# Performance work log

Measured on AMD Instinct MI355X. Metric: run time of the kernel, lower is better.

The kernel has to match this reference:

```python
import jax, jax.numpy as jnp
import numpy as np
from jax import lax

B_, L_, D_, N_, K_ = 2, 4096, 1024, 16, 4


def setup_inputs() -> dict:
    key = jax.random.key(0)
    ks = jax.random.split(key, 11)
    s = lambda fan: 1.0 / np.sqrt(fan)
    return {
        "x": jax.random.normal(ks[0], (B_, L_, D_), jnp.float32),
        "W_in": jax.random.normal(ks[1], (D_, 2 * D_), jnp.float32) * s(D_),
        "b_in": jax.random.normal(ks[2], (2 * D_,), jnp.float32) * 0.01,
        "conv_w": jax.random.normal(ks[3], (D_, K_), jnp.float32) * s(K_),
        "conv_b": jax.random.normal(ks[4], (D_,), jnp.float32) * 0.01,
        "W_x": jax.random.normal(ks[5], (D_, 2 * N_), jnp.float32) * s(D_),
        "b_x": jax.random.normal(ks[6], (2 * N_,), jnp.float32) * 0.01,
        "A_log": jax.random.normal(ks[7], (D_, N_), jnp.float32),
        "D_param": jnp.ones((D_,), jnp.float32),
        "W_out": jax.random.normal(ks[8], (D_, D_), jnp.float32) * s(D_),
        "b_out": jax.random.normal(ks[9], (D_,), jnp.float32) * 0.01,
    }


def silu(x):
    return x * jax.nn.sigmoid(x)


def s6_forward(x, W_in, b_in, conv_w, conv_b, W_x, b_x, A_log, D_param, W_out, b_out):
    b, L, D = x.shape
    # in_proj then split into ssm stream and gate
    x_and_gate = x @ W_in + b_in                      # [b, L, 2D]
    x_ssm, gate = jnp.split(x_and_gate, 2, axis=-1)   # each [b, L, D]

    # depthwise causal conv: padding=(d_conv-1, d_conv-1) then [:, :, :L] == left-pad only
    xc = jnp.transpose(x_ssm, (0, 2, 1))              # [b, D, L]
    xc = lax.conv_general_dilated(
        xc, conv_w[:, None, :],                       # [D, 1, K]
        window_strides=(1,), padding=[(K_ - 1, 0)],
        feature_group_count=D,
        dimension_numbers=("NCH", "OIH", "NCH"),
    ) + conv_b[None, :, None]
    x_conv = silu(jnp.transpose(xc, (0, 2, 1)))       # [b, L, D]

    # data-dependent B, C
    BC = x_conv @ W_x + b_x                           # [b, L, 2N]
    B_mat, C_mat = jnp.split(BC, 2, axis=-1)          # each [b, L, N]

    A_discrete = jnp.exp(-jnp.exp(A_log))             # [D, N]

    # sequential selective scan over L, carry h: [b, D, N]
    def step(h, inp):
        xc_t, B_t, C_t = inp                          # [b,D], [b,N], [b,N]
        h = A_discrete[None] * h + xc_t[:, :, None] * B_t[:, None, :]
        y = jnp.einsum("bn,bdn->bd", C_t, h) + D_param * xc_t
        return h, y

    h0 = jnp.zeros((b, D, N_), x.dtype)
    xs = (jnp.transpose(x_conv, (1, 0, 2)),
          jnp.transpose(B_mat, (1, 0, 2)),
          jnp.transpose(C_mat, (1, 0, 2)))
    h_final, ys = lax.scan(step, h0, xs)              # ys: [L, b, D]
    y = jnp.transpose(ys, (1, 0, 2))                  # [b, L, D]

    y = y * silu(gate)
    y = y @ W_out + b_out
    final_state = h_final.mean(axis=1)                # [b, N]
    return y, final_state


def reference(x, W_in, b_in, conv_w, conv_b, W_x, b_x, A_log, D_param, W_out, b_out):
    return s6_forward(x, W_in, b_in, conv_w, conv_b, W_x, b_x, A_log, D_param, W_out, b_out)
```

## Files before the change

kernel.cpp:

```cpp
#include <hip/hip_runtime.h>
#include <hip/hip_bf16.h>
#include <math.h>

#define LL 4096
#define DD 1024
#define NN 16
#define KK 4
#define BB 2
#define MM (BB * LL)
#define NC 128
#define LC 32

typedef unsigned short ushort_t;
typedef short s16x8 __attribute__((ext_vector_type(8)));
typedef float f32x4 __attribute__((ext_vector_type(4)));
typedef unsigned int u32;

__device__ __forceinline__ ushort_t f2bf(float f) {
  __hip_bfloat16 h = __float2bfloat16(f);
  return *reinterpret_cast<ushort_t*>(&h);
}
__device__ __forceinline__ float bf2f(ushort_t u) {
  union { u32 i; float f; } c;
  c.i = ((u32)u) << 16;
  return c.f;
}

template <bool BF16OUT>
__global__ __launch_bounds__(256) void gemm_bt_mfma(
    const ushort_t* __restrict__ A,
    const ushort_t* __restrict__ BT,
    const float* __restrict__ bias,
    void* __restrict__ Cv, int N) {
  constexpr int K = 1024;
  __shared__ ushort_t As[128 * 64];
  __shared__ ushort_t Bs[128 * 64];

  const int tid = threadIdx.x;
  const int lane = tid & 63;
  const int w = tid >> 6;
  const int wm = w & 1, wn = w >> 1;
  const int row0 = blockIdx.y * 128;
  const int col0 = blockIdx.x * 128;

  const int lrow8 = lane >> 3;
  const int lkc = (lane & 7) ^ lrow8;

  f32x4 acc[4][4];
#pragma unroll
  for (int i = 0; i < 4; ++i)
#pragma unroll
    for (int j = 0; j < 4; ++j) acc[i][j] = (f32x4){0.f, 0.f, 0.f, 0.f};

  const int frow = lane & 15;
  const int quad = lane >> 4;
  const int r7 = frow & 7;

  for (int k0 = 0; k0 < K; k0 += 64) {
#pragma unroll
    for (int it = 0; it < 4; ++it) {
      int r = it * 32 + w * 8;
      __builtin_amdgcn_global_load_lds(
          (const __attribute__((address_space(1))) u32*)(A + (size_t)(row0 + r + lrow8) * K + k0 + lkc * 8),
          (__attribute__((address_space(3))) u32*)(As + r * 64), 16, 0, 0);
      __builtin_amdgcn_global_load_lds(
          (const __attribute__((address_space(1))) u32*)(BT + (size_t)(col0 + r + lrow8) * K + k0 + lkc * 8),
          (__attribute__((address_space(3))) u32*)(Bs + r * 64), 16, 0, 0);
    }
    __syncthreads();

#pragma unroll
    for (int half = 0; half < 2; ++half) {
      s16x8 af[4], bf[4];
#pragma unroll
      for (int mi = 0; mi < 4; ++mi)
        af[mi] = *(const s16x8*)&As[(wm * 64 + mi * 16 + frow) * 64 +
                                    (((half * 4 + quad) ^ r7) * 8)];
#pragma unroll
      for (int ni = 0; ni < 4; ++ni)
        bf[ni] = *(const s16x8*)&Bs[(wn * 64 + ni * 16 + frow) * 64 +
                                    (((half * 4 + quad) ^ r7) * 8)];
#pragma unroll
      for (int mi = 0; mi < 4; ++mi)
#pragma unroll
        for (int ni = 0; ni < 4; ++ni)
          acc[mi][ni] = __builtin_amdgcn_mfma_f32_16x16x32_bf16(
              af[mi], bf[ni], acc[mi][ni], 0, 0, 0);
    }
    __syncthreads();
  }

#pragma unroll
  for (int mi = 0; mi < 4; ++mi) {
#pragma unroll
    for (int ni = 0; ni < 4; ++ni) {
      int col = col0 + wn * 64 + ni * 16 + frow;
      float b = bias[col];
#pragma unroll
      for (int r = 0; r < 4; ++r) {
        int row = row0 + wm * 64 + mi * 16 + quad * 4 + r;
        if constexpr (BF16OUT)
          ((ushort_t*)Cv)[(size_t)row * N + col] = f2bf(acc[mi][ni][r] + b);
        else
          ((float*)Cv)[(size_t)row * N + col] = acc[mi][ni][r] + b;
      }
    }
  }
}

__global__ __launch_bounds__(128) void bc_mfma_k(
    const ushort_t* __restrict__ A, const ushort_t* __restrict__ BT,
    const float* __restrict__ bias, float* __restrict__ C) {
  constexpr int K = 1024;
  __shared__ ushort_t As[32 * 32];
  __shared__ ushort_t Bs[32 * 32];

  const int tid = threadIdx.x;
  const int lane = tid & 63;
  const int w = tid >> 6;
  const int row0 = blockIdx.x * 32;
  const int lrow = lane >> 2;
  const int lkc = (lane & 3) ^ ((lrow >> 1) & 3);
  const int frow = lane & 15;
  const int quad = lane >> 4;
  const int sw = (frow >> 1) & 3;

  f32x4 acc[2];
  acc[0] = (f32x4){0.f, 0.f, 0.f, 0.f};
  acc[1] = (f32x4){0.f, 0.f, 0.f, 0.f};

  for (int k0 = 0; k0 < K; k0 += 32) {
    __builtin_amdgcn_global_load_lds(
        (const __attribute__((address_space(1))) u32*)(A + (size_t)(row0 + w * 16 + lrow) * K + k0 + lkc * 8),
        (__attribute__((address_space(3))) u32*)(As + (w * 16) * 32), 16, 0, 0);
    __builtin_amdgcn_global_load_lds(
        (const __attribute__((address_space(1))) u32*)(BT + (size_t)(w * 16 + lrow) * K + k0 + lkc * 8),
        (__attribute__((address_space(3))) u32*)(Bs + (w * 16) * 32), 16, 0, 0);
    __syncthreads();

    s16x8 af = *(const s16x8*)&As[(w * 16 + frow) * 32 + (quad ^ sw) * 8];
    s16x8 bf0 = *(const s16x8*)&Bs[(frow)*32 + (quad ^ sw) * 8];
    s16x8 bf1 = *(const s16x8*)&Bs[(16 + frow) * 32 + (quad ^ sw) * 8];
    acc[0] = __builtin_amdgcn_mfma_f32_16x16x32_bf16(af, bf0, acc[0], 0, 0, 0);
    acc[1] = __builtin_amdgcn_mfma_f32_16x16x32_bf16(af, bf1, acc[1], 0, 0, 0);
    __syncthreads();
  }

#pragma unroll
  for (int ni = 0; ni < 2; ++ni) {
    int col = ni * 16 + frow;
    float b = bias[col];
#pragma unroll
    for (int r = 0; r < 4; ++r) {
      int row = row0 + w * 16 + quad * 4 + r;
      C[(size_t)row * 32 + col] = acc[ni][r] + b;
    }
  }
}

__global__ __launch_bounds__(256) void prep_k(
    const float* __restrict__ x, ushort_t* __restrict__ Xb,
    float* __restrict__ fs, const float* __restrict__ W_in,
    const float* __restrict__ W_out, const float* __restrict__ W_x,
    ushort_t* __restrict__ WinT, ushort_t* __restrict__ WoutT,
    ushort_t* __restrict__ WxT, const float* __restrict__ A_log,
    float* __restrict__ Adis, float* __restrict__ ALC) {
  constexpr int K = 1024;
  const int tid = threadIdx.x;
  if (blockIdx.z == 0) {
    if (blockIdx.x == 0 && blockIdx.y == 0 && tid < 32) fs[tid] = 0.f;
    int i = (blockIdx.y * 64 + blockIdx.x) * 256 + tid;
    float4 v = ((const float4*)x)[i];
    ushort4 o;
    o.x = f2bf(v.x); o.y = f2bf(v.y); o.z = f2bf(v.z); o.w = f2bf(v.w);
    ((ushort4*)Xb)[i] = o;
    return;
  }
  int by = blockIdx.y;
  if (by >= 96) {
    if (by >= 104 || blockIdx.x != 0) return;
    int base = (by - 96) * 2048 + tid * 8;
#pragma unroll
    for (int j = 0; j < 8; ++j) {
      float e = __expf(A_log[base + j]);
      Adis[base + j] = __expf(-e);
      ALC[base + j] = __expf(-(float)LC * e);
    }
    return;
  }
  const float* W;
  ushort_t* WT;
  int N;
  if (by < 32) {
    W = W_in; WT = WinT; N = 2048;
  } else if (by < 64) {
    if (blockIdx.x >= 32) return;
    W = W_out; WT = WoutT; N = 1024;
    by -= 32;
  } else {
    if (blockIdx.x >= 1) return;
    W = W_x; WT = WxT; N = 32;
    by -= 64;
  }
  __shared__ float t[32][33];
  int nb = blockIdx.x * 32, kb = by * 32;
  int tx = tid & 31, ty = tid >> 5;
#pragma unroll
  for (int i = 0; i < 32; i += 8)
    t[ty + i][tx] = W[(size_t)(kb + ty + i) * N + nb + tx];
  __syncthreads();
#pragma unroll
  for (int i = 0; i < 32; i += 8)
    WT[(size_t)(nb + ty + i) * K + kb + tx] = f2bf(t[tx][ty + i]);
}

__global__ __launch_bounds__(256) void conv_silu_k(
    const ushort_t* __restrict__ XGb, const float* __restrict__ conv_w,
    const float* __restrict__ conv_b, ushort_t* __restrict__ XCb) {
  __shared__ float cw[128 * 33];
  const int tid = threadIdx.x;
#pragma unroll
  for (int j = 0; j < 4; ++j) {
    int d = tid + j * 256;
    float4 v = ((const float4*)conv_w)[d];
    float* p = &cw[(d >> 3) * 33 + (d & 7) * 4];
    p[0] = v.x; p[1] = v.y; p[2] = v.z; p[3] = v.w;
  }
  __syncthreads();

  int gid = blockIdx.x * 256 + tid;
  int m = gid >> 7;
  int dg = gid & 127;
  int d0 = dg * 8;
  int l = m & (LL - 1);
  const float* w = &cw[dg * 33];

  float4 b0 = ((const float4*)conv_b)[dg * 2];
  float4 b1 = ((const float4*)conv_b)[dg * 2 + 1];
  float acc[8] = {b0.x, b0.y, b0.z, b0.w, b1.x, b1.y, b1.z, b1.w};

#pragma unroll
  for (int k = 0; k < KK; ++k) {
    int li = l + k - (KK - 1);
    if (li < 0) continue;
    s16x8 v = *(const s16x8*)(XGb + (size_t)(m + k - (KK - 1)) * 2048 + d0);
#pragma unroll
    for (int j = 0; j < 8; ++j)
      acc[j] += bf2f((ushort_t)v[j]) * w[j * 4 + k];
  }
  ushort_t o[8];
#pragma unroll
  for (int j = 0; j < 8; ++j) {
    float s = acc[j] / (1.f + __expf(-acc[j]));
    o[j] = f2bf(s);
  }
  *(s16x8*)(XCb + (size_t)m * DD + d0) = *(const s16x8*)o;
}

__global__ __launch_bounds__(256) void scan_local_k(
    const ushort_t* __restrict__ XCb, const float* __restrict__ BC,
    const float* __restrict__ Adis, float* __restrict__ S) {
  const int b = blockIdx.x;
  const int w = threadIdx.x >> 6;
  const int lane = threadIdx.x & 63;
  const int c = blockIdx.y * 4 + w;
  const int d0 = blockIdx.z * 128 + lane * 2;
  const int t0 = c * LC;
  const size_t rowb = (size_t)b * LL;

  __shared__ float bcs_all[4][LC * 32];
  float* bcs = bcs_all[w];
  {
    const float4* src = (const float4*)(BC + (rowb + t0) * 32);
    float4* dst = (float4*)bcs;
#pragma unroll
    for (int i = 0; i < 4; ++i) dst[lane + i * 64] = src[lane + i * 64];
  }
  f32x4 av[8];
#pragma unroll
  for (int i = 0; i < 8; ++i) av[i] = *(const f32x4*)(Adis + d0 * 16 + i * 4);

  float h0[NN], h1[NN];
#pragma unroll
  for (int n = 0; n < NN; ++n) { h0[n] = 0.f; h1[n] = 0.f; }

  const ushort_t* xp = XCb + (rowb + t0) * DD + d0;
  u32 xw = *(const u32*)xp;
  for (int t = 0; t < LC; ++t) {
    u32 xw_n = (t + 1 < LC) ? *(const u32*)(xp + (size_t)(t + 1) * DD) : 0u;
    float x0 = bf2f((ushort_t)(xw & 0xffff));
    float x1 = bf2f((ushort_t)(xw >> 16));
    const float* bp = bcs + t * 32;
#pragma unroll
    for (int n = 0; n < NN; ++n) {
      float bv = bp[n];
      h0[n] = av[n >> 2][n & 3] * h0[n] + x0 * bv;
      h1[n] = av[4 + (n >> 2)][n & 3] * h1[n] + x1 * bv;
    }
    xw = xw_n;
  }
  float* sp = S + ((size_t)(b * NC + c) * NN) * DD + d0;
#pragma unroll
  for (int n = 0; n < NN; ++n) {
    float2 v = {h0[n], h1[n]};
    *(float2*)(sp + (size_t)n * DD) = v;
  }
}

__global__ __launch_bounds__(256) void scan_carry_k(
    float* __restrict__ S, const float* __restrict__ ALC,
    float* __restrict__ fs) {
  const int idx = blockIdx.x * 256 + threadIdx.x;
  const int d = idx & (DD - 1);
  const int n = (idx >> 10) & (NN - 1);
  const int b = idx >> 14;

  const float aLC = ALC[d * NN + n];
  float h = 0.f;
  for (int c = 0; c < NC; ++c) {
    size_t off = ((size_t)(b * NC + c) * NN + n) * DD + d;
    float s = S[off];
    S[off] = h;
    h = aLC * h + s;
  }
  __shared__ float red[256];
  red[threadIdx.x] = h;
  __syncthreads();
#pragma unroll
  for (int s2 = 128; s2 > 0; s2 >>= 1) {
    if (threadIdx.x < s2) red[threadIdx.x] += red[threadIdx.x + s2];
    __syncthreads();
  }
  if (threadIdx.x == 0) atomicAdd(&fs[b * NN + n], red[0] * (1.f / (float)DD));
}

__global__ __launch_bounds__(256) void scan_final_k(
    const ushort_t* __restrict__ XCb, const ushort_t* __restrict__ XGb,
    const float* __restrict__ BC, const float* __restrict__ Adis,
    const float* __restrict__ D_param, const float* __restrict__ H0,
    ushort_t* __restrict__ Y1b) {
  const int b = blockIdx.x;
  const int w = threadIdx.x >> 6;
  const int lane = threadIdx.x & 63;
  const int c = blockIdx.y * 4 + w;
  const int d0 = blockIdx.z * 128 + lane * 2;
  const int t0 = c * LC;
  const size_t rowb = (size_t)b * LL;

  __shared__ float bcs_all[4][LC * 32];
  float* bcs = bcs_all[w];
  {
    const float4* src = (const float4*)(BC + (rowb + t0) * 32);
    float4* dst = (float4*)bcs;
#pragma unroll
    for (int i = 0; i < 4; ++i) dst[lane + i * 64] = src[lane + i * 64];
  }
  f32x4 av[8];
#pragma unroll
  for (int i = 0; i < 8; ++i) av[i] = *(const f32x4*)(Adis + d0 * 16 + i * 4);

  float h0[NN], h1[NN];
  const float* hp = H0 + ((size_t)(b * NC + c) * NN) * DD + d0;
#pragma unroll
  for (int n = 0; n < NN; ++n) {
    float2 v = *(const float2*)(hp + (size_t)n * DD);
    h0[n] = v.x;
    h1[n] = v.y;
  }
  float2 Dp = *(const float2*)(D_param + d0);

  const ushort_t* xp = XCb + (rowb + t0) * DD + d0;
  const ushort_t* gp = XGb + (rowb + t0) * 2048 + DD + d0;
  ushort_t* yp = Y1b + (rowb + t0) * DD + d0;
  u32 xw = *(const u32*)xp;
  u32 gw = *(const u32*)gp;
  for (int t = 0; t < LC; ++t) {
    u32 xw_n = 0u, gw_n = 0u;
    if (t + 1 < LC) {
      xw_n = *(const u32*)(xp + (size_t)(t + 1) * DD);
      gw_n = *(const u32*)(gp + (size_t)(t + 1) * 2048);
    }
    float x0 = bf2f((ushort_t)(xw & 0xffff));
    float x1 = bf2f((ushort_t)(xw >> 16));
    float g0 = bf2f((ushort_t)(gw & 0xffff));
    float g1 = bf2f((ushort_t)(gw >> 16));
    float y0 = Dp.x * x0, y1 = Dp.y * x1;
    const float* bp = bcs + t * 32;
#pragma unroll
    for (int n = 0; n < NN; ++n) {
      float bv = bp[n], cv = bp[16 + n];
      h0[n] = av[n >> 2][n & 3] * h0[n] + x0 * bv;
      h1[n] = av[4 + (n >> 2)][n & 3] * h1[n] + x1 * bv;
      y0 += cv * h0[n];
      y1 += cv * h1[n];
    }
    float sg0 = g0 / (1.f + __expf(-g0));
    float sg1 = g1 / (1.f + __expf(-g1));
    u32 outw = (u32)f2bf(y0 * sg0) | ((u32)f2bf(y1 * sg1) << 16);
    *(u32*)(yp + (size_t)t * DD) = outw;
    xw = xw_n;
    gw = gw_n;
  }
}

extern "C" void kernel_launch(void* const* d_in, const int* in_sizes, int n_in,
                              void* d_out, int out_size, void* d_ws,
                              size_t ws_size, hipStream_t stream) {
  const float* x = (const float*)d_in[0];
  const float* W_in = (const float*)d_in[1];
  const float* b_in = (const float*)d_in[2];
  const float* conv_w = (const float*)d_in[3];
  const float* conv_b = (const float*)d_in[4];
  const float* W_x = (const float*)d_in[5];
  const float* b_x = (const float*)d_in[6];
  const float* A_log = (const float*)d_in[7];
  const float* D_param = (const float*)d_in[8];
  const float* W_out = (const float*)d_in[9];
  const float* b_out = (const float*)d_in[10];
  float* out = (float*)d_out;
  float* fs = out + (size_t)MM * DD;

  float* BC = (float*)d_ws;
  float* S = BC + (size_t)MM * 32;
  float* Adis = S + (size_t)BB * NC * NN * DD;
  float* ALC = Adis + (size_t)DD * NN;
  ushort_t* Xb = (ushort_t*)(ALC + (size_t)DD * NN);
  ushort_t* XGb = Xb + (size_t)MM * DD;
  ushort_t* XCb = XGb + (size_t)MM * 2048;
  ushort_t* Y1b = XCb + (size_t)MM * DD;
  ushort_t* WinT = Y1b + (size_t)MM * DD;
  ushort_t* WoutT = WinT + (size_t)2048 * DD;
  ushort_t* WxT = WoutT + (size_t)DD * DD;

  dim3 blk(256);
  prep_k<<<dim3(64, 128, 2), blk, 0, stream>>>(x, Xb, fs, W_in, W_out, W_x,
                                               WinT, WoutT, WxT, A_log, Adis,
                                               ALC);
  gemm_bt_mfma<true><<<dim3(2048 / 128, MM / 128), blk, 0, stream>>>(
      Xb, WinT, b_in, XGb, 2048);
  conv_silu_k<<<dim3((MM * 128) / 256), blk, 0, stream>>>(XGb, conv_w, conv_b,
                                                          XCb);
  bc_mfma_k<<<dim3(MM / 32), dim3(128), 0, stream>>>(XCb, WxT, b_x, BC);
  scan_local_k<<<dim3(BB, NC / 4, DD / 128), blk, 0, stream>>>(XCb, BC, Adis,
                                                               S);
  scan_carry_k<<<dim3((BB * DD * NN) / 256), blk, 0, stream>>>(S, ALC, fs);
  scan_final_k<<<dim3(BB, NC / 4, DD / 128), blk, 0, stream>>>(
      XCb, XGb, BC, Adis, D_param, S, Y1b);
  gemm_bt_mfma<false><<<dim3(1024 / 128, MM / 128), blk, 0, stream>>>(
      Y1b, WoutT, b_out, out, 1024);
}
```

Before: 249.7 us.

## Fuse causal conv+SiLU into BC GEMM and scan kernels, drop XCb buffer

Removes the standalone conv_silu kernel and the bf16 XCb intermediate. The BC projection kernel now computes conv+SiLU on the fly into LDS before its MFMA, and both scan kernels recompute conv+SiLU from XGb using a sliding 4-tap register window. This cuts one launch and a write plus several reads of an 8M×bf16 buffer, at the cost of redundant conv arithmetic and strided loads from the wider XGb rows. The carry scan also prefetches the next chunk value.

```diff
diff --git a/kernel.cpp b/kernel.cpp
--- a/kernel.cpp
+++ b/kernel.cpp
@@ -24,6 +24,9 @@
   union { u32 i; float f; } c;
   c.i = ((u32)u) << 16;
   return c.f;
+}
+__device__ __forceinline__ float silu(float v) {
+  return v / (1.f + __expf(-v));
 }
 
 template <bool BF16OUT>
@@ -108,53 +111,91 @@
   }
 }
 
-__global__ __launch_bounds__(128) void bc_mfma_k(
-    const ushort_t* __restrict__ A, const ushort_t* __restrict__ BT,
-    const float* __restrict__ bias, float* __restrict__ C) {
+__global__ __launch_bounds__(256) void convbc_k(
+    const ushort_t* __restrict__ XGb,
+    const float* __restrict__ conv_w,
+    const float* __restrict__ conv_b,
+    const ushort_t* __restrict__ WxT,
+    const float* __restrict__ b_x,
+    float* __restrict__ BC) {
   constexpr int K = 1024;
-  __shared__ ushort_t As[32 * 32];
-  __shared__ ushort_t Bs[32 * 32];
+  __shared__ ushort_t As[32 * 64];
+  __shared__ ushort_t Bs[32 * 64];
+  __shared__ float cw[128 * 33];
+  __shared__ float cb[1024];
 
   const int tid = threadIdx.x;
   const int lane = tid & 63;
   const int w = tid >> 6;
+  const int wm = w & 1, wn = w >> 1;
   const int row0 = blockIdx.x * 32;
-  const int lrow = lane >> 2;
-  const int lkc = (lane & 3) ^ ((lrow >> 1) & 3);
+  const int l0 = row0 & (LL - 1);
+
+#pragma unroll
+  for (int j = 0; j < 4; ++j) {
+    int d = tid + j * 256;
+    float4 v = ((const float4*)conv_w)[d];
+    float* p = &cw[(d >> 3) * 33 + (d & 7) * 4];
+    p[0] = v.x; p[1] = v.y; p[2] = v.z; p[3] = v.w;
+    cb[d] = conv_b[d];
+  }
+  __syncthreads();
+
+  const int r = tid >> 3;
+  const int o = tid & 7;
+  const int l = l0 + r;
   const int frow = lane & 15;
   const int quad = lane >> 4;
-  const int sw = (frow >> 1) & 3;
-
-  f32x4 acc[2];
-  acc[0] = (f32x4){0.f, 0.f, 0.f, 0.f};
-  acc[1] = (f32x4){0.f, 0.f, 0.f, 0.f};
-
-  for (int k0 = 0; k0 < K; k0 += 32) {
+  const int lkc = (lane & 7) ^ (lane >> 3);
+
+  f32x4 acc = (f32x4){0.f, 0.f, 0.f, 0.f};
+
+  for (int kk = 0; kk < K; kk += 64) {
+    const ushort_t* xb = XGb + (size_t)(row0 + r) * 2048 + kk + o * 8;
+    s16x8 v[4];
+#pragma unroll
+    for (int k = 0; k < 4; ++k) {
+      if (l + k - 3 >= 0)
+        v[k] = *(const s16x8*)(xb + (ptrdiff_t)(k - 3) * 2048);
+      else
+        v[k] = (s16x8){0, 0, 0, 0, 0, 0, 0, 0};
+    }
+    const int dg = (kk >> 3) + o;
+    const float* wp = &cw[dg * 33];
+    float a8[8];
+#pragma unroll
+    for (int j = 0; j < 8; ++j) a8[j] = cb[kk + o * 8 + j];
+#pragma unroll
+    for (int k = 0; k < 4; ++k)
+#pragma unroll
+      for (int j = 0; j < 8; ++j)
+        a8[j] += bf2f((ushort_t)v[k][j]) * wp[j * 4 + k];
+    ushort_t pk[8];
+#pragma unroll
+    for (int j = 0; j < 8; ++j) pk[j] = f2bf(silu(a8[j]));
+    *(s16x8*)&As[r * 64 + (o ^ (r & 7)) * 8] = *(const s16x8*)pk;
+
     __builtin_amdgcn_global_load_lds(
-        (const __attribute__((address_space(1))) u32*)(A + (size_t)(row0 + w * 16 + lrow) * K + k0 + lkc * 8),
-        (__attribute__((address_space(3))) u32*)(As + (w * 16) * 32), 16, 0, 0);
-    __builtin_amdgcn_global_load_lds(
-        (const __attribute__((address_space(1))) u32*)(BT + (size_t)(w * 16 + lrow) * K + k0 + lkc * 8),
-        (__attribute__((address_space(3))) u32*)(Bs + (w * 16) * 32), 16, 0, 0);
+        (const __attribute__((address_space(1))) u32*)(WxT + (size_t)(w * 8 + (lane >> 3)) * 1024 + kk + lkc * 8),
+        (__attribute__((address_space(3))) u32*)(Bs + (w * 8 + (lane >> 3)) * 64), 16, 0, 0);
     __syncthreads();
 
-    s16x8 af = *(const s16x8*)&As[(w * 16 + frow) * 32 + (quad ^ sw) * 8];
-    s16x8 bf0 = *(const s16x8*)&Bs[(frow)*32 + (quad ^ sw) * 8];
-    s16x8 bf1 = *(const s16x8*)&Bs[(16 + frow) * 32 + (quad ^ sw) * 8];
-    acc[0] = __builtin_amdgcn_mfma_f32_16x16x32_bf16(af, bf0, acc[0], 0, 0, 0);
-    acc[1] = __builtin_amdgcn_mfma_f32_16x16x32_bf16(af, bf1, acc[1], 0, 0, 0);
+#pragma unroll
+    for (int s = 0; s < 2; ++s) {
+      int slot = ((s * 4 + quad) ^ (frow & 7)) * 8;
+      s16x8 af = *(const s16x8*)&As[(wm * 16 + frow) * 64 + slot];
+      s16x8 bf = *(const s16x8*)&Bs[(wn * 16 + frow) * 64 + slot];
+      acc = __builtin_amdgcn_mfma_f32_16x16x32_bf16(af, bf, acc, 0, 0, 0);
+    }
     __syncthreads();
   }
 
-#pragma unroll
-  for (int ni = 0; ni < 2; ++ni) {
-    int col = ni * 16 + frow;
-    float b = bias[col];
-#pragma unroll
-    for (int r = 0; r < 4; ++r) {
-      int row = row0 + w * 16 + quad * 4 + r;
-      C[(size_t)row * 32 + col] = acc[ni][r] + b;
-    }
+  int col = wn * 16 + frow;
+  float b = b_x[col];
+#pragma unroll
+  for (int rr = 0; rr < 4; ++rr) {
+    int row = row0 + wm * 16 + quad * 4 + rr;
+    BC[(size_t)row * 32 + col] = acc[rr] + b;
   }
 }
 
@@ -214,52 +255,10 @@
     WT[(size_t)(nb + ty + i) * K + kb + tx] = f2bf(t[tx][ty + i]);
 }
 
-__global__ __launch_bounds__(256) void conv_silu_k(
-    const ushort_t* __restrict__ XGb, const float* __restrict__ conv_w,
-    const float* __restrict__ conv_b, ushort_t* __restrict__ XCb) {
-  __shared__ float cw[128 * 33];
-  const int tid = threadIdx.x;
-#pragma unroll
-  for (int j = 0; j < 4; ++j) {
-    int d = tid + j * 256;
-    float4 v = ((const float4*)conv_w)[d];
-    float* p = &cw[(d >> 3) * 33 + (d & 7) * 4];
-    p[0] = v.x; p[1] = v.y; p[2] = v.z; p[3] = v.w;
-  }
-  __syncthreads();
-
-  int gid = blockIdx.x * 256 + tid;
-  int m = gid >> 7;
-  int dg = gid & 127;
-  int d0 = dg * 8;
-  int l = m & (LL - 1);
-  const float* w = &cw[dg * 33];
-
-  float4 b0 = ((const float4*)conv_b)[dg * 2];
-  float4 b1 = ((const float4*)conv_b)[dg * 2 + 1];
-  float acc[8] = {b0.x, b0.y, b0.z, b0.w, b1.x, b1.y, b1.z, b1.w};
-
-#pragma unroll
-  for (int k = 0; k < KK; ++k) {
-    int li = l + k - (KK - 1);
-    if (li < 0) continue;
-    s16x8 v = *(const s16x8*)(XGb + (size_t)(m + k - (KK - 1)) * 2048 + d0);
-#pragma unroll
-    for (int j = 0; j < 8; ++j)
-      acc[j] += bf2f((ushort_t)v[j]) * w[j * 4 + k];
-  }
-  ushort_t o[8];
-#pragma unroll
-  for (int j = 0; j < 8; ++j) {
-    float s = acc[j] / (1.f + __expf(-acc[j]));
-    o[j] = f2bf(s);
-  }
-  *(s16x8*)(XCb + (size_t)m * DD + d0) = *(const s16x8*)o;
-}
-
 __global__ __launch_bounds__(256) void scan_local_k(
-    const ushort_t* __restrict__ XCb, const float* __restrict__ BC,
-    const float* __restrict__ Adis, float* __restrict__ S) {
+    const ushort_t* __restrict__ XGb, const float* __restrict__ BC,
+    const float* __restrict__ Adis, const float* __restrict__ conv_w,
+    const float* __restrict__ conv_b, float* __restrict__ S) {
   const int b = blockIdx.x;
   const int w = threadIdx.x >> 6;
   const int lane = threadIdx.x & 63;
@@ -279,17 +278,32 @@
   f32x4 av[8];
 #pragma unroll
   for (int i = 0; i < 8; ++i) av[i] = *(const f32x4*)(Adis + d0 * 16 + i * 4);
+  float4 w0 = ((const float4*)conv_w)[d0];
+  float4 w1 = ((const float4*)conv_w)[d0 + 1];
+  float2 cb2 = *(const float2*)(conv_b + d0);
 
   float h0[NN], h1[NN];
 #pragma unroll
   for (int n = 0; n < NN; ++n) { h0[n] = 0.f; h1[n] = 0.f; }
 
-  const ushort_t* xp = XCb + (rowb + t0) * DD + d0;
-  u32 xw = *(const u32*)xp;
+  const ushort_t* xbase = XGb + rowb * 2048 + d0;
+  u32 win[4];
+#pragma unroll
+  for (int k = 0; k < 4; ++k) {
+    int l = t0 - 3 + k;
+    win[k] = (l >= 0) ? *(const u32*)(xbase + (size_t)l * 2048) : 0u;
+  }
   for (int t = 0; t < LC; ++t) {
-    u32 xw_n = (t + 1 < LC) ? *(const u32*)(xp + (size_t)(t + 1) * DD) : 0u;
-    float x0 = bf2f((ushort_t)(xw & 0xffff));
-    float x1 = bf2f((ushort_t)(xw >> 16));
+    u32 win_n = (t + 1 < LC) ? *(const u32*)(xbase + (size_t)(t0 + t + 1) * 2048) : 0u;
+    float v0 = cb2.x, v1 = cb2.y;
+#pragma unroll
+    for (int k = 0; k < 4; ++k) {
+      float wk0 = (k == 0) ? w0.x : (k == 1) ? w0.y : (k == 2) ? w0.z : w0.w;
+      float wk1 = (k == 0) ? w1.x : (k == 1) ? w1.y : (k == 2) ? w1.z : w1.w;
+      v0 += bf2f((ushort_t)(win[k] & 0xffff)) * wk0;
+      v1 += bf2f((ushort_t)(win[k] >> 16)) * wk1;
+    }
+    float x0 = silu(v0), x1 = silu(v1);
     const float* bp = bcs + t * 32;
 #pragma unroll
     for (int n = 0; n < NN; ++n) {
@@ -297,7 +311,7 @@
       h0[n] = av[n >> 2][n & 3] * h0[n] + x0 * bv;
       h1[n] = av[4 + (n >> 2)][n & 3] * h1[n] + x1 * bv;
     }
-    xw = xw_n;
+    win[0] = win[1]; win[1] = win[2]; win[2] = win[3]; win[3] = win_n;
   }
   float* sp = S + ((size_t)(b * NC + c) * NN) * DD + d0;
 #pragma unroll
@@ -316,12 +330,15 @@
   const int b = idx >> 14;
 
   const float aLC = ALC[d * NN + n];
+  const size_t base = ((size_t)b * NC * NN + n) * DD + d;
+  const size_t step = (size_t)NN * DD;
   float h = 0.f;
+  float s = S[base];
   for (int c = 0; c < NC; ++c) {
-    size_t off = ((size_t)(b * NC + c) * NN + n) * DD + d;
-    float s = S[off];
-    S[off] = h;
+    float s_n = (c + 1 < NC) ? S[base + (size_t)(c + 1) * step] : 0.f;
+    S[base + (size_t)c * step] = h;
     h = aLC * h + s;
+    s = s_n;
   }
   __shared__ float red[256];
   red[threadIdx.x] = h;
@@ -335,10 +352,10 @@
 }
 
 __global__ __launch_bounds__(256) void scan_final_k(
-    const ushort_t* __restrict__ XCb, const ushort_t* __restrict__ XGb,
-    const float* __restrict__ BC, const float* __restrict__ Adis,
-    const float* __restrict__ D_param, const float* __restrict__ H0,
-    ushort_t* __restrict__ Y1b) {
+    const ushort_t* __restrict__ XGb, const float* __restrict__ BC,
+    const float* __restrict__ Adis, const float* __restrict__ conv_w,
+    const float* __restrict__ conv_b, const float* __restrict__ D_param,
+    const float* __restrict__ H0, ushort_t* __restrict__ Y1b) {
   const int b = blockIdx.x;
   const int w = threadIdx.x >> 6;
   const int lane = threadIdx.x & 63;
@@ -358,6 +375,9 @@
   f32x4 av[8];
 #pragma unroll
   for (int i = 0; i < 8; ++i) av[i] = *(const f32x4*)(Adis + d0 * 16 + i * 4);
+  float4 w0 = ((const float4*)conv_w)[d0];
+  float4 w1 = ((const float4*)conv_w)[d0 + 1];
+  float2 cb2 = *(const float2*)(conv_b + d0);
 
   float h0[NN], h1[NN];
   const float* hp = H0 + ((size_t)(b * NC + c) * NN) * DD + d0;
@@ -369,19 +389,31 @@
   }
   float2 Dp = *(const float2*)(D_param + d0);
 
-  const ushort_t* xp = XCb + (rowb + t0) * DD + d0;
-  const ushort_t* gp = XGb + (rowb + t0) * 2048 + DD + d0;
+  const ushort_t* xbase = XGb + rowb * 2048 + d0;
+  const ushort_t* gbase = XGb + rowb * 2048 + DD + d0;
   ushort_t* yp = Y1b + (rowb + t0) * DD + d0;
-  u32 xw = *(const u32*)xp;
-  u32 gw = *(const u32*)gp;
+  u32 win[4];
+#pragma unroll
+  for (int k = 0; k < 4; ++k) {
+    int l = t0 - 3 + k;
+    win[k] = (l >= 0) ? *(const u32*)(xbase + (size_t)l * 2048) : 0u;
+  }
+  u32 gw = *(const u32*)(gbase + (size_t)t0 * 2048);
   for (int t = 0; t < LC; ++t) {
-    u32 xw_n = 0u, gw_n = 0u;
+    u32 win_n = 0u, gw_n = 0u;
     if (t + 1 < LC) {
-      xw_n = *(const u32*)(xp + (size_t)(t + 1) * DD);
-      gw_n = *(const u32*)(gp + (size_t)(t + 1) * 2048);
-    }
-    float x0 = bf2f((ushort_t)(xw & 0xffff));
-    float x1 = bf2f((ushort_t)(xw >> 16));
+      win_n = *(const u32*)(xbase + (size_t)(t0 + t + 1) * 2048);
+      gw_n = *(const u32*)(gbase + (size_t)(t0 + t + 1) * 2048);
+    }
+    float v0 = cb2.x, v1 = cb2.y;
+#pragma unroll
+    for (int k = 0; k < 4; ++k) {
+      float wk0 = (k == 0) ? w0.x : (k == 1) ? w0.y : (k == 2) ? w0.z : w0.w;
+      float wk1 = (k == 0) ? w1.x : (k == 1) ? w1.y : (k == 2) ? w1.z : w1.w;
+      v0 += bf2f((ushort_t)(win[k] & 0xffff)) * wk0;
+      v1 += bf2f((ushort_t)(win[k] >> 16)) * wk1;
+    }
+    float x0 = silu(v0), x1 = silu(v1);
     float g0 = bf2f((ushort_t)(gw & 0xffff));
     float g1 = bf2f((ushort_t)(gw >> 16));
     float y0 = Dp.x * x0, y1 = Dp.y * x1;
@@ -394,11 +426,9 @@
       y0 += cv * h0[n];
       y1 += cv * h1[n];
     }
-    float sg0 = g0 / (1.f + __expf(-g0));
-    float sg1 = g1 / (1.f + __expf(-g1));
-    u32 outw = (u32)f2bf(y0 * sg0) | ((u32)f2bf(y1 * sg1) << 16);
+    u32 outw = (u32)f2bf(y0 * silu(g0)) | ((u32)f2bf(y1 * silu(g1)) << 16);
     *(u32*)(yp + (size_t)t * DD) = outw;
-    xw = xw_n;
+    win[0] = win[1]; win[1] = win[2]; win[2] = win[3]; win[3] = win_n;
     gw = gw_n;
   }
 }
@@ -426,8 +456,7 @@
   float* ALC = Adis + (size_t)DD * NN;
   ushort_t* Xb = (ushort_t*)(ALC + (size_t)DD * NN);
   ushort_t* XGb = Xb + (size_t)MM * DD;
-  ushort_t* XCb = XGb + (size_t)MM * 2048;
-  ushort_t* Y1b = XCb + (size_t)MM * DD;
+  ushort_t* Y1b = XGb + (size_t)MM * 2048;
   ushort_t* WinT = Y1b + (size_t)MM * DD;
   ushort_t* WoutT = WinT + (size_t)2048 * DD;
   ushort_t* WxT = WoutT + (size_t)DD * DD;
@@ -438,14 +467,13 @@
                                                ALC);
   gemm_bt_mfma<true><<<dim3(2048 / 128, MM / 128), blk, 0, stream>>>(
       Xb, WinT, b_in, XGb, 2048);
-  conv_silu_k<<<dim3((MM * 128) / 256), blk, 0, stream>>>(XGb, conv_w, conv_b,
-                                                          XCb);
-  bc_mfma_k<<<dim3(MM / 32), dim3(128), 0, stream>>>(XCb, WxT, b_x, BC);
-  scan_local_k<<<dim3(BB, NC / 4, DD / 128), blk, 0, stream>>>(XCb, BC, Adis,
-                                                               S);
+  convbc_k<<<dim3(MM / 32), blk, 0, stream>>>(XGb, conv_w, conv_b, WxT, b_x,
+                                              BC);
+  scan_local_k<<<dim3(BB, NC / 4, DD / 128), blk, 0, stream>>>(
+      XGb, BC, Adis, conv_w, conv_b, S);
   scan_carry_k<<<dim3((BB * DD * NN) / 256), blk, 0, stream>>>(S, ALC, fs);
   scan_final_k<<<dim3(BB, NC / 4, DD / 128), blk, 0, stream>>>(
-      XCb, XGb, BC, Adis, D_param, S, Y1b);
+      XGb, BC, Adis, conv_w, conv_b, D_param, S, Y1b);
   gemm_bt_mfma<false><<<dim3(1024 / 128, MM / 128), blk, 0, stream>>>(
       Y1b, WoutT, b_out, out, 1024);
 }
```

Result: slower. 260.4 us (+4.3%).
